# Performance work log

Measured on AMD Instinct MI355X. Metric: run time of the kernel, lower is better.

## Reference

```python
import jax, jax.numpy as jnp
import numpy as np

N = 131072
H = 768

def setup_inputs() -> dict:
    key = jax.random.key(0)
    k1, k2, k3, k4 = jax.random.split(key, 4)
    h_i = jax.random.normal(k1, (N, H), dtype=jnp.float32)
    W_weight = jax.random.normal(k2, (H, H), dtype=jnp.float32) * 0.02
    W_bias = jax.random.normal(k3, (H,), dtype=jnp.float32) * 0.02
    v = jax.random.normal(k4, (1, H), dtype=jnp.float32) * 0.1
    return {"h_i": h_i, "W_weight": W_weight, "W_bias": W_bias, "v": v}

def reference(h_i, W_weight, W_bias, v):
    # u_i = tanh(Linear(h_i)) : [N, H]
    u_i = jnp.tanh(h_i @ W_weight.T + W_bias)
    # scores = v @ u_i.T : [1, N]
    scores = v @ u_i.T
    alpha = jax.nn.softmax(scores, axis=1)  # [1, N]
    # weighted sum over N -> [1, H]
    return alpha @ h_i
```

## Files before the change

kernel.cpp:

```cpp
#include <hip/hip_runtime.h>

#define HDIM 768
#define BM 64
#define NCHUNK 24
#define CHUNK_B 49152
#define A_STRIDE 1536
#define ASWZ(row) (((row) & 7) << 4)

typedef _Float16 f16x8 __attribute__((ext_vector_type(8)));
typedef _Float16 f16x4 __attribute__((ext_vector_type(4)));
typedef float f32x4 __attribute__((ext_vector_type(4)));

#define LDS_A     0
#define LDS_BB    98304
#define LDS_BIAS  147456
#define LDS_V     150528
#define LDS_SRED  153600
#define LDS_E     157696
#define LDS_TOTAL 157952

#define WS_WT    0
#define WS_Z     1179648
#define WS_PART  1179712
#define WS_PART2 7471168
#define WS_NEED  (WS_PART2 + 49152)

__device__ __forceinline__ float tanh_fast(float z) {
    float e2 = __expf(2.0f * z);
    return 1.0f - 2.0f / (e2 + 1.0f);
}

__device__ __forceinline__ void stage16(const void* g, void* l) {
    __builtin_amdgcn_global_load_lds(
        (const __attribute__((address_space(1))) void*)g,
        (__attribute__((address_space(3))) void*)l, 16, 0, 0);
}

__device__ __forceinline__ f16x8 cvt8(f32x4 x0, f32x4 x1) {
    f16x8 f;
    f[0] = (_Float16)x0[0]; f[1] = (_Float16)x0[1];
    f[2] = (_Float16)x0[2]; f[3] = (_Float16)x0[3];
    f[4] = (_Float16)x1[0]; f[5] = (_Float16)x1[1];
    f[6] = (_Float16)x1[2]; f[7] = (_Float16)x1[3];
    return f;
}

__global__ __launch_bounds__(1024) void prep_kernel(
    const float* __restrict__ W, _Float16* __restrict__ Wt,
    float* __restrict__ Z, float* __restrict__ accbuf) {
    int idx = blockIdx.x * 1024 + threadIdx.x;
    if (idx < 73728) {
        int c  = idx / 96;
        int r  = idx - c * 96;
        int kc = r >> 2;
        int q  = r & 3;
        const float* src = W + c * HDIM + kc * 32 + q * 8;
        f32x4 x0 = *(const f32x4*)src;
        f32x4 x1 = *(const f32x4*)(src + 4);
        f16x8 v = cvt8(x0, x1);
        int qs = q ^ ((c >> 1) & 3);
        *(f16x8*)((char*)Wt + (size_t)kc * CHUNK_B + c * 64 + qs * 16) = v;
    }
    if (idx < HDIM) accbuf[idx] = 0.0f;
    if (idx == 0) *Z = 0.0f;
}

__global__ __launch_bounds__(1024, 4) void score_fused_kernel(
    const float* __restrict__ h, const _Float16* __restrict__ Wt,
    const float* __restrict__ bias, const float* __restrict__ vvec,
    float* __restrict__ part, float* __restrict__ accbuf,
    float* __restrict__ Z, int use_part) {

    extern __shared__ char smem[];
    float* bias_s = (float*)(smem + LDS_BIAS);
    float* v_s    = (float*)(smem + LDS_V);
    float* s_red  = (float*)(smem + LDS_SRED);
    float* e_lds  = (float*)(smem + LDS_E);

    const int tid  = threadIdx.x;
    const int wave = tid >> 6;
    const int lane = tid & 63;
    const int l15  = lane & 15;
    const int lhi  = lane >> 4;
    const int row0 = blockIdx.x * BM;

    if (tid < HDIM) { bias_s[tid] = bias[tid]; v_s[tid] = vvec[tid]; }

    const int quad = lhi ^ ((l15 >> 1) & 3);
    const int boff = (wave * 48 + l15) * 64 + quad * 16;

    #pragma unroll
    for (int s = 0; s < 3; ++s) {
        int idx = wave * 3 + s;
        stage16((const char*)Wt + idx * 1024 + lane * 16, smem + LDS_BB + idx * 1024);
    }
    if (tid < 512) {
        int r = tid >> 3, k4 = tid & 7;
        f32x4 x = *(const f32x4*)(h + (size_t)(row0 + r) * HDIM + k4 * 4);
        f16x4 v;
        v[0] = (_Float16)x[0]; v[1] = (_Float16)x[1];
        v[2] = (_Float16)x[2]; v[3] = (_Float16)x[3];
        *(f16x4*)(smem + LDS_A + r * A_STRIDE + ((k4 * 8) ^ ASWZ(r))) = v;
    }
    __syncthreads();

    f32x4 acc[4][3];
    #pragma unroll
    for (int rt = 0; rt < 4; ++rt)
        #pragma unroll
        for (int ct = 0; ct < 3; ++ct)
            acc[rt][ct] = (f32x4){0.f, 0.f, 0.f, 0.f};

    const int aswz = ASWZ(l15);

    for (int kc = 0; kc < NCHUNK; ++kc) {
        const bool has = (kc + 1 < NCHUNK);
        f32x4 pa;
        if (has && tid < 512)
            pa = *(const f32x4*)(h + (size_t)(row0 + (tid >> 3)) * HDIM
                                   + (kc + 1) * 32 + (tid & 7) * 4);

        const char* bb = smem + LDS_BB + boff;
        f16x8 b0 = *(const f16x8*)(bb);
        f16x8 b1 = *(const f16x8*)(bb + 1024);
        f16x8 b2 = *(const f16x8*)(bb + 2048);
        const char* ab = smem + LDS_A + l15 * A_STRIDE + ((kc * 64 + lhi * 16) ^ aswz);
        f16x8 a0 = *(const f16x8*)(ab);
        f16x8 a1 = *(const f16x8*)(ab + 16 * A_STRIDE);
        f16x8 a2 = *(const f16x8*)(ab + 32 * A_STRIDE);
        f16x8 a3 = *(const f16x8*)(ab + 48 * A_STRIDE);
        acc[0][0] = __builtin_amdgcn_mfma_f32_16x16x32_f16(a0, b0, acc[0][0], 0, 0, 0);
        acc[0][1] = __builtin_amdgcn_mfma_f32_16x16x32_f16(a0, b1, acc[0][1], 0, 0, 0);
        acc[0][2] = __builtin_amdgcn_mfma_f32_16x16x32_f16(a0, b2, acc[0][2], 0, 0, 0);
        acc[1][0] = __builtin_amdgcn_mfma_f32_16x16x32_f16(a1, b0, acc[1][0], 0, 0, 0);
        acc[1][1] = __builtin_amdgcn_mfma_f32_16x16x32_f16(a1, b1, acc[1][1], 0, 0, 0);
        acc[1][2] = __builtin_amdgcn_mfma_f32_16x16x32_f16(a1, b2, acc[1][2], 0, 0, 0);
        acc[2][0] = __builtin_amdgcn_mfma_f32_16x16x32_f16(a2, b0, acc[2][0], 0, 0, 0);
        acc[2][1] = __builtin_amdgcn_mfma_f32_16x16x32_f16(a2, b1, acc[2][1], 0, 0, 0);
        acc[2][2] = __builtin_amdgcn_mfma_f32_16x16x32_f16(a2, b2, acc[2][2], 0, 0, 0);
        acc[3][0] = __builtin_amdgcn_mfma_f32_16x16x32_f16(a3, b0, acc[3][0], 0, 0, 0);
        acc[3][1] = __builtin_amdgcn_mfma_f32_16x16x32_f16(a3, b1, acc[3][1], 0, 0, 0);
        acc[3][2] = __builtin_amdgcn_mfma_f32_16x16x32_f16(a3, b2, acc[3][2], 0, 0, 0);

        __syncthreads();

        if (has) {
            const char* g = (const char*)Wt + (size_t)(kc + 1) * CHUNK_B;
            #pragma unroll
            for (int s = 0; s < 3; ++s) {
                int idx = wave * 3 + s;
                stage16(g + idx * 1024 + lane * 16, smem + LDS_BB + idx * 1024);
            }
            if (tid < 512) {
                int r = tid >> 3;
                f16x4 v;
                v[0] = (_Float16)pa[0]; v[1] = (_Float16)pa[1];
                v[2] = (_Float16)pa[2]; v[3] = (_Float16)pa[3];
                *(f16x4*)(smem + LDS_A + r * A_STRIDE
                          + (((kc + 1) * 64 + (tid & 7) * 8) ^ ASWZ(r))) = v;
            }
        }
        __syncthreads();
    }

    float pr[4][4];
    #pragma unroll
    for (int rt = 0; rt < 4; ++rt)
        #pragma unroll
        for (int r = 0; r < 4; ++r) pr[rt][r] = 0.f;

    #pragma unroll
    for (int ct = 0; ct < 3; ++ct) {
        int col = wave * 48 + ct * 16 + l15;
        float bj = bias_s[col];
        float vj = v_s[col];
        #pragma unroll
        for (int rt = 0; rt < 4; ++rt)
            #pragma unroll
            for (int r = 0; r < 4; ++r)
                pr[rt][r] = fmaf(vj, tanh_fast(acc[rt][ct][r] + bj), pr[rt][r]);
    }
    #pragma unroll
    for (int rt = 0; rt < 4; ++rt)
        #pragma unroll
        for (int r = 0; r < 4; ++r) {
            float x = pr[rt][r];
            x += __shfl_xor(x, 1);
            x += __shfl_xor(x, 2);
            x += __shfl_xor(x, 4);
            x += __shfl_xor(x, 8);
            if (l15 == 0) s_red[wave * 64 + rt * 16 + lhi * 4 + r] = x;
        }
    __syncthreads();

    if (tid < 64) {
        float s = 0.f;
        #pragma unroll
        for (int w = 0; w < 16; ++w) s += s_red[w * 64 + tid];
        float e = __expf(s);
        e_lds[tid] = e;
        float tot = e;
        tot += __shfl_xor(tot, 1);
        tot += __shfl_xor(tot, 2);
        tot += __shfl_xor(tot, 4);
        tot += __shfl_xor(tot, 8);
        tot += __shfl_xor(tot, 16);
        tot += __shfl_xor(tot, 32);
        if (tid == 0) atomicAdd(Z, tot);
    }
    __syncthreads();

    if (tid < HDIM) {
        float s = 0.f;
        #pragma unroll 8
        for (int i = 0; i < BM; ++i) {
            const _Float16* ap = (const _Float16*)(smem + LDS_A + i * A_STRIDE
                                                   + ((tid * 2) ^ ASWZ(i)));
            s += e_lds[i] * (float)(*ap);
        }
        if (use_part) part[(size_t)blockIdx.x * HDIM + tid] = s;
        else          atomicAdd(accbuf + tid, s);
    }
}

__global__ __launch_bounds__(128) void fin1_kernel(
    const float* __restrict__ part, float* __restrict__ part2) {
    const int g  = blockIdx.x / 6;
    const int cb = blockIdx.x % 6;
    const int col = cb * 128 + threadIdx.x;
    float s = 0.f;
    #pragma unroll 8
    for (int p = g * 128; p < (g + 1) * 128; ++p) s += part[(size_t)p * HDIM + col];
    part2[g * HDIM + col] = s;
}

__global__ __launch_bounds__(128) void fin2_kernel(
    const float* __restrict__ src, const float* __restrict__ Z,
    float* __restrict__ out, int ngroups) {
    const int col = blockIdx.x * 128 + threadIdx.x;
    float s = 0.f;
    for (int g = 0; g < ngroups; ++g) s += src[g * HDIM + col];
    out[col] = s / (*Z);
}

extern "C" void kernel_launch(void* const* d_in, const int* in_sizes, int n_in,
                              void* d_out, int out_size, void* d_ws, size_t ws_size,
                              hipStream_t stream) {
    const float* h    = (const float*)d_in[0];
    const float* W    = (const float*)d_in[1];
    const float* bias = (const float*)d_in[2];
    const float* vv   = (const float*)d_in[3];
    float* out = (float*)d_out;

    const int n = in_sizes[0] / HDIM;

    char* ws = (char*)d_ws;
    _Float16* Wt  = (_Float16*)(ws + WS_WT);
    float* Z      = (float*)(ws + WS_Z);
    float* part   = (float*)(ws + WS_PART);
    float* part2  = (float*)(ws + WS_PART2);
    float* accbuf = (float*)(ws + WS_PART);

    const int use_part = (ws_size >= (size_t)WS_NEED) ? 1 : 0;

    hipFuncSetAttribute((const void*)score_fused_kernel,
                        hipFuncAttributeMaxDynamicSharedMemorySize, LDS_TOTAL);

    prep_kernel<<<72, 1024, 0, stream>>>(W, Wt, Z, accbuf);

    score_fused_kernel<<<n / BM, 1024, LDS_TOTAL, stream>>>(
        h, Wt, bias, vv, part, accbuf, Z, use_part);

    if (use_part) {
        fin1_kernel<<<96, 128, 0, stream>>>(part, part2);
        fin2_kernel<<<HDIM / 128, 128, 0, stream>>>(part2, Z, out, 16);
    } else {
        fin2_kernel<<<HDIM / 128, 128, 0, stream>>>(accbuf, Z, out, 1);
    }
}
```

Measured before the change: 328.7 us.

## Load W tiles directly into registers and double-buffer with a single barrier

Removes the LDS staging buffer for the f16 weight tiles. Each wave now loads its B fragments straight from global memory into registers, double-buffered one chunk ahead, and h is prefetched two chunks ahead with nontemporal loads. The two __syncthreads per chunk become one waitcnt-plus-barrier, and the loop is unrolled by two so the register buffers ping-pong. This cuts LDS use and barrier overhead, but it depends on global/L2 latency for the B operand and on the A-buffer writes for chunk k+1 not racing with reads of chunk k.

```diff
diff --git a/kernel.cpp b/kernel.cpp
--- a/kernel.cpp
+++ b/kernel.cpp
@@ -3,7 +3,7 @@
 #define HDIM 768
 #define BM 64
 #define NCHUNK 24
-#define CHUNK_B 49152
+#define CHALF 24576
 #define A_STRIDE 1536
 #define ASWZ(row) (((row) & 7) << 4)
 
@@ -12,12 +12,11 @@
 typedef float f32x4 __attribute__((ext_vector_type(4)));
 
 #define LDS_A     0
-#define LDS_BB    98304
-#define LDS_BIAS  147456
-#define LDS_V     150528
-#define LDS_SRED  153600
-#define LDS_E     157696
-#define LDS_TOTAL 157952
+#define LDS_BIAS  98304
+#define LDS_V     101376
+#define LDS_SRED  104448
+#define LDS_E     108544
+#define LDS_TOTAL 108800
 
 #define WS_WT    0
 #define WS_Z     1179648
@@ -28,12 +27,6 @@
 __device__ __forceinline__ float tanh_fast(float z) {
     float e2 = __expf(2.0f * z);
     return 1.0f - 2.0f / (e2 + 1.0f);
-}
-
-__device__ __forceinline__ void stage16(const void* g, void* l) {
-    __builtin_amdgcn_global_load_lds(
-        (const __attribute__((address_space(1))) void*)g,
-        (__attribute__((address_space(3))) void*)l, 16, 0, 0);
 }
 
 __device__ __forceinline__ f16x8 cvt8(f32x4 x0, f32x4 x1) {
@@ -55,11 +48,8 @@
         int kc = r >> 2;
         int q  = r & 3;
         const float* src = W + c * HDIM + kc * 32 + q * 8;
-        f32x4 x0 = *(const f32x4*)src;
-        f32x4 x1 = *(const f32x4*)(src + 4);
-        f16x8 v = cvt8(x0, x1);
-        int qs = q ^ ((c >> 1) & 3);
-        *(f16x8*)((char*)Wt + (size_t)kc * CHUNK_B + c * 64 + qs * 16) = v;
+        f16x8 v = cvt8(*(const f32x4*)src, *(const f32x4*)(src + 4));
+        *(f16x8*)(Wt + (size_t)kc * CHALF + c * 32 + q * 8) = v;
     }
     if (idx < HDIM) accbuf[idx] = 0.0f;
     if (idx == 0) *Z = 0.0f;
@@ -86,22 +76,26 @@
 
     if (tid < HDIM) { bias_s[tid] = bias[tid]; v_s[tid] = vvec[tid]; }
 
-    const int quad = lhi ^ ((l15 >> 1) & 3);
-    const int boff = (wave * 48 + l15) * 64 + quad * 16;
-
-    #pragma unroll
-    for (int s = 0; s < 3; ++s) {
-        int idx = wave * 3 + s;
-        stage16((const char*)Wt + idx * 1024 + lane * 16, smem + LDS_BB + idx * 1024);
-    }
+    const _Float16* wtp = Wt + (wave * 48 + l15) * 32 + lhi * 8;
+    const int aswz = ASWZ(l15);
+
     if (tid < 512) {
         int r = tid >> 3, k4 = tid & 7;
-        f32x4 x = *(const f32x4*)(h + (size_t)(row0 + r) * HDIM + k4 * 4);
+        f32x4 x = __builtin_nontemporal_load(
+            (const f32x4*)(h + (size_t)(row0 + r) * HDIM + k4 * 4));
         f16x4 v;
         v[0] = (_Float16)x[0]; v[1] = (_Float16)x[1];
         v[2] = (_Float16)x[2]; v[3] = (_Float16)x[3];
         *(f16x4*)(smem + LDS_A + r * A_STRIDE + ((k4 * 8) ^ ASWZ(r))) = v;
     }
+    f32x4 paA = {0.f, 0.f, 0.f, 0.f}, paB = {0.f, 0.f, 0.f, 0.f};
+    if (tid < 512)
+        paA = __builtin_nontemporal_load(
+            (const f32x4*)(h + (size_t)(row0 + (tid >> 3)) * HDIM + 32 + (tid & 7) * 4));
+    f16x8 bA0 = *(const f16x8*)(wtp);
+    f16x8 bA1 = *(const f16x8*)(wtp + 512);
+    f16x8 bA2 = *(const f16x8*)(wtp + 1024);
+    f16x8 bB0, bB1, bB2;
     __syncthreads();
 
     f32x4 acc[4][3];
@@ -111,57 +105,54 @@
         for (int ct = 0; ct < 3; ++ct)
             acc[rt][ct] = (f32x4){0.f, 0.f, 0.f, 0.f};
 
-    const int aswz = ASWZ(l15);
-
-    for (int kc = 0; kc < NCHUNK; ++kc) {
-        const bool has = (kc + 1 < NCHUNK);
-        f32x4 pa;
-        if (has && tid < 512)
-            pa = *(const f32x4*)(h + (size_t)(row0 + (tid >> 3)) * HDIM
-                                   + (kc + 1) * 32 + (tid & 7) * 4);
-
-        const char* bb = smem + LDS_BB + boff;
-        f16x8 b0 = *(const f16x8*)(bb);
-        f16x8 b1 = *(const f16x8*)(bb + 1024);
-        f16x8 b2 = *(const f16x8*)(bb + 2048);
-        const char* ab = smem + LDS_A + l15 * A_STRIDE + ((kc * 64 + lhi * 16) ^ aswz);
-        f16x8 a0 = *(const f16x8*)(ab);
-        f16x8 a1 = *(const f16x8*)(ab + 16 * A_STRIDE);
-        f16x8 a2 = *(const f16x8*)(ab + 32 * A_STRIDE);
-        f16x8 a3 = *(const f16x8*)(ab + 48 * A_STRIDE);
-        acc[0][0] = __builtin_amdgcn_mfma_f32_16x16x32_f16(a0, b0, acc[0][0], 0, 0, 0);
-        acc[0][1] = __builtin_amdgcn_mfma_f32_16x16x32_f16(a0, b1, acc[0][1], 0, 0, 0);
-        acc[0][2] = __builtin_amdgcn_mfma_f32_16x16x32_f16(a0, b2, acc[0][2], 0, 0, 0);
-        acc[1][0] = __builtin_amdgcn_mfma_f32_16x16x32_f16(a1, b0, acc[1][0], 0, 0, 0);
-        acc[1][1] = __builtin_amdgcn_mfma_f32_16x16x32_f16(a1, b1, acc[1][1], 0, 0, 0);
-        acc[1][2] = __builtin_amdgcn_mfma_f32_16x16x32_f16(a1, b2, acc[1][2], 0, 0, 0);
-        acc[2][0] = __builtin_amdgcn_mfma_f32_16x16x32_f16(a2, b0, acc[2][0], 0, 0, 0);
-        acc[2][1] = __builtin_amdgcn_mfma_f32_16x16x32_f16(a2, b1, acc[2][1], 0, 0, 0);
-        acc[2][2] = __builtin_amdgcn_mfma_f32_16x16x32_f16(a2, b2, acc[2][2], 0, 0, 0);
-        acc[3][0] = __builtin_amdgcn_mfma_f32_16x16x32_f16(a3, b0, acc[3][0], 0, 0, 0);
-        acc[3][1] = __builtin_amdgcn_mfma_f32_16x16x32_f16(a3, b1, acc[3][1], 0, 0, 0);
-        acc[3][2] = __builtin_amdgcn_mfma_f32_16x16x32_f16(a3, b2, acc[3][2], 0, 0, 0);
-
-        __syncthreads();
-
-        if (has) {
-            const char* g = (const char*)Wt + (size_t)(kc + 1) * CHUNK_B;
-            #pragma unroll
-            for (int s = 0; s < 3; ++s) {
-                int idx = wave * 3 + s;
-                stage16(g + idx * 1024 + lane * 16, smem + LDS_BB + idx * 1024);
-            }
-            if (tid < 512) {
-                int r = tid >> 3;
-                f16x4 v;
-                v[0] = (_Float16)pa[0]; v[1] = (_Float16)pa[1];
-                v[2] = (_Float16)pa[2]; v[3] = (_Float16)pa[3];
-                *(f16x4*)(smem + LDS_A + r * A_STRIDE
-                          + (((kc + 1) * 64 + (tid & 7) * 8) ^ ASWZ(r))) = v;
-            }
-        }
-        __syncthreads();
-    }
+#define CHUNK(KC, BC0, BC1, BC2, BN0, BN1, BN2, PAW, PAL)                              \
+    {                                                                                   \
+        const char* ab = smem + LDS_A + l15 * A_STRIDE + (((KC) * 64 + lhi * 16) ^ aswz); \
+        f16x8 a0 = *(const f16x8*)(ab);                                                 \
+        f16x8 a1 = *(const f16x8*)(ab + 16 * A_STRIDE);                                 \
+        f16x8 a2 = *(const f16x8*)(ab + 32 * A_STRIDE);                                 \
+        f16x8 a3 = *(const f16x8*)(ab + 48 * A_STRIDE);                                 \
+        if ((KC) + 1 < NCHUNK) {                                                        \
+            const _Float16* wp = wtp + (size_t)((KC) + 1) * CHALF;                      \
+            BN0 = *(const f16x8*)(wp);                                                  \
+            BN1 = *(const f16x8*)(wp + 512);                                            \
+            BN2 = *(const f16x8*)(wp + 1024);                                           \
+        }                                                                               \
+        if ((KC) + 2 < NCHUNK && tid < 512)                                             \
+            PAL = __builtin_nontemporal_load(                                           \
+                (const f32x4*)(h + (size_t)(row0 + (tid >> 3)) * HDIM                   \
+                               + ((KC) + 2) * 32 + (tid & 7) * 4));                     \
+        acc[0][0] = __builtin_amdgcn_mfma_f32_16x16x32_f16(a0, BC0, acc[0][0], 0, 0, 0); \
+        acc[0][1] = __builtin_amdgcn_mfma_f32_16x16x32_f16(a0, BC1, acc[0][1], 0, 0, 0); \
+        acc[0][2] = __builtin_amdgcn_mfma_f32_16x16x32_f16(a0, BC2, acc[0][2], 0, 0, 0); \
+        acc[1][0] = __builtin_amdgcn_mfma_f32_16x16x32_f16(a1, BC0, acc[1][0], 0, 0, 0); \
+        acc[1][1] = __builtin_amdgcn_mfma_f32_16x16x32_f16(a1, BC1, acc[1][1], 0, 0, 0); \
+        acc[1][2] = __builtin_amdgcn_mfma_f32_16x16x32_f16(a1, BC2, acc[1][2], 0, 0, 0); \
+        acc[2][0] = __builtin_amdgcn_mfma_f32_16x16x32_f16(a2, BC0, acc[2][0], 0, 0, 0); \
+        acc[2][1] = __builtin_amdgcn_mfma_f32_16x16x32_f16(a2, BC1, acc[2][1], 0, 0, 0); \
+        acc[2][2] = __builtin_amdgcn_mfma_f32_16x16x32_f16(a2, BC2, acc[2][2], 0, 0, 0); \
+        acc[3][0] = __builtin_amdgcn_mfma_f32_16x16x32_f16(a3, BC0, acc[3][0], 0, 0, 0); \
+        acc[3][1] = __builtin_amdgcn_mfma_f32_16x16x32_f16(a3, BC1, acc[3][1], 0, 0, 0); \
+        acc[3][2] = __builtin_amdgcn_mfma_f32_16x16x32_f16(a3, BC2, acc[3][2], 0, 0, 0); \
+        if ((KC) + 1 < NCHUNK && tid < 512) {                                           \
+            int r_ = tid >> 3;                                                          \
+            f16x4 v_;                                                                   \
+            v_[0] = (_Float16)PAW[0]; v_[1] = (_Float16)PAW[1];                         \
+            v_[2] = (_Float16)PAW[2]; v_[3] = (_Float16)PAW[3];                         \
+            *(f16x4*)(smem + LDS_A + r_ * A_STRIDE                                      \
+                      + ((((KC) + 1) * 64 + (tid & 7) * 8) ^ ASWZ(r_))) = v_;           \
+        }                                                                               \
+        asm volatile("s_waitcnt lgkmcnt(0)" ::: "memory");                              \
+        __builtin_amdgcn_s_barrier();                                                   \
+    }
+
+    for (int k2 = 0; k2 < NCHUNK; k2 += 2) {
+        CHUNK(k2,     bA0, bA1, bA2, bB0, bB1, bB2, paA, paB)
+        CHUNK(k2 + 1, bB0, bB1, bB2, bA0, bA1, bA2, paB, paA)
+    }
+#undef CHUNK
+
+    __syncthreads();
 
     float pr[4][4];
     #pragma unroll
```

New measurement: 288.6 us. 1.14x faster.
